# Kernel optimization log

Hardware: AMD Instinct MI355X
Metric: run time of the kernel (lower is better)

The kernel has to match this reference:

```python
import jax, jax.numpy as jnp
import numpy as np

TOPK = 5
POWER = 1.01


def setup_inputs() -> dict:
    key = jax.random.key(0)
    k1, k2 = jax.random.split(key)
    B, C = 16384, 8192
    inp = jax.random.normal(k1, (B, C), dtype=jnp.float32)
    target = jax.random.randint(k2, (B,), 0, C, dtype=jnp.int64 if jax.config.jax_enable_x64 else jnp.int32)
    return {"input": inp, "target": target}


def reference(input, target):
    B = input.shape[0]
    rows = jnp.arange(B)
    # log(softmax(x)) == log_softmax(x)
    log_prob = jax.nn.log_softmax(input, axis=-1)  # [B, C]
    # top-k selection over classes
    topk_vals, topk_idx = jax.lax.top_k(input, TOPK)  # [B, K]
    # custom power-based softmax on the top-k subset
    exp_in = jnp.power(jnp.asarray(POWER, input.dtype), topk_vals)  # [B, K]
    log_prob_topk = jnp.log(exp_in / jnp.sum(exp_in, axis=-1, keepdims=True))
    # scatter the top-k log-probs back into a copy of log_prob
    log_prob_copy = log_prob.at[rows[:, None], topk_idx].set(log_prob_topk)
    # gather-based cross-entropy terms
    loss1 = jnp.mean(-log_prob[rows, target])
    loss2 = jnp.mean(-log_prob_copy[rows, target])
    return loss1 + loss2
```

## Files before the change

### kernel.cpp

```cpp
#include <hip/hip_runtime.h>

#define BLOCK 256
#define NCHUNK 8
#define NC 8192

typedef float f4 __attribute__((ext_vector_type(4)));

__device__ __forceinline__ float fexp2(float x) { return __builtin_amdgcn_exp2f(x); }
__device__ __forceinline__ float flog2(float x) { return __builtin_amdgcn_logf(x); }

__device__ __forceinline__ void cas(float& hi, float& lo) {
    float h = fmaxf(hi, lo), l = fminf(hi, lo);
    hi = h; lo = l;
}

__device__ __forceinline__ void sort5(float& a0, float& a1, float& a2, float& a3, float& a4) {
    cas(a0, a1); cas(a3, a4); cas(a2, a4); cas(a2, a3); cas(a1, a4);
    cas(a0, a3); cas(a0, a2); cas(a1, a3); cas(a1, a2);
}

__device__ __forceinline__ void merge55(float& a0, float& a1, float& a2, float& a3, float& a4,
                                        float b0, float b1, float b2, float b3, float b4) {
    float L0 = fmaxf(a0, b4);
    float L1 = fmaxf(a1, b3);
    float L2 = fmaxf(a2, b2);
    float L3 = fmaxf(a3, b1);
    float L4 = fmaxf(a4, b0);
    sort5(L0, L1, L2, L3, L4);
    a0 = L0; a1 = L1; a2 = L2; a3 = L3; a4 = L4;
}

__global__ __launch_bounds__(BLOCK, 6) void ce_topk_rows(const float* __restrict__ inp,
                                                         const int* __restrict__ target,
                                                         float* __restrict__ row_loss) {
    constexpr float LOG2E  = 1.4426950408889634f;
    constexpr float LN2    = 0.6931471805599453f;
    constexpr float LN_P   = 0.009950330853155723f;
    constexpr float LOG2_P = 0.014355292977070041f;
    const float NI = -__builtin_inff();

    const int row  = blockIdx.x;
    const int tid  = threadIdx.x;
    const int lane = tid & 63;
    const int wav  = tid >> 6;
    const float* rp = inp + (size_t)row * NC;

    __shared__ float wsum[4];
    __shared__ float wtop[4][5];

    float xt = 0.f;
    if (tid == 0) xt = rp[target[row]];

    f4 c[NCHUNK];
    #pragma unroll
    for (int j = 0; j < NCHUNK; ++j)
        c[j] = reinterpret_cast<const f4*>(rp)[tid + BLOCK * j];

    float es = 0.f;
    float a0, a1, a2, a3, a4;

    {
        float v0 = c[0][0], v1 = c[0][1], v2 = c[0][2], v3 = c[0][3];
        es = (fexp2(v0 * LOG2E) + fexp2(v1 * LOG2E))
           + (fexp2(v2 * LOG2E) + fexp2(v3 * LOG2E));
        cas(v0, v1); cas(v2, v3); cas(v0, v2); cas(v1, v3); cas(v1, v2);
        a0 = v0; a1 = v1; a2 = v2; a3 = v3; a4 = NI;
    }

    #pragma unroll
    for (int j = 1; j < NCHUNK; ++j) {
        float v0 = c[j][0], v1 = c[j][1], v2 = c[j][2], v3 = c[j][3];
        es += (fexp2(v0 * LOG2E) + fexp2(v1 * LOG2E))
            + (fexp2(v2 * LOG2E) + fexp2(v3 * LOG2E));
        cas(v0, v1); cas(v2, v3); cas(v0, v2); cas(v1, v3); cas(v1, v2);
        a1 = fmaxf(a1, v3);
        a2 = fmaxf(a2, v2);
        a3 = fmaxf(a3, v1);
        a4 = fmaxf(a4, v0);
        sort5(a0, a1, a2, a3, a4);
    }

    #pragma unroll
    for (int o = 32; o > 0; o >>= 1) es += __shfl_xor(es, o, 64);

    #pragma unroll
    for (int o = 1; o < 64; o <<= 1) {
        float b0 = __shfl_xor(a0, o, 64);
        float b1 = __shfl_xor(a1, o, 64);
        float b2 = __shfl_xor(a2, o, 64);
        float b3 = __shfl_xor(a3, o, 64);
        float b4 = __shfl_xor(a4, o, 64);
        merge55(a0, a1, a2, a3, a4, b0, b1, b2, b3, b4);
    }

    if (lane == 0) {
        wsum[wav] = es;
        wtop[wav][0] = a0; wtop[wav][1] = a1; wtop[wav][2] = a2;
        wtop[wav][3] = a3; wtop[wav][4] = a4;
    }
    __syncthreads();

    if (tid == 0) {
        float s = wsum[0] + wsum[1] + wsum[2] + wsum[3];
        float A0 = wtop[0][0], A1 = wtop[0][1], A2 = wtop[0][2], A3 = wtop[0][3], A4 = wtop[0][4];
        #pragma unroll
        for (int w = 1; w < 4; ++w)
            merge55(A0, A1, A2, A3, A4,
                    wtop[w][0], wtop[w][1], wtop[w][2], wtop[w][3], wtop[w][4]);

        float spsum = fexp2(A0 * LOG2_P) + fexp2(A1 * LOG2_P) + fexp2(A2 * LOG2_P)
                    + fexp2(A3 * LOG2_P) + fexp2(A4 * LOG2_P);

        float lse  = LN2 * flog2(s);
        float l1   = lse - xt;
        float lsep = LN2 * flog2(spsum);
        bool found = (xt >= A4);
        float l2   = found ? (lsep - xt * LN_P) : l1;
        row_loss[row] = l1 + l2;
    }
}

__global__ __launch_bounds__(1024) void ce_topk_reduce(const float* __restrict__ rl,
                                                       float* __restrict__ out, int B) {
    float acc = 0.f;
    const float4* r4 = (const float4*)rl;
    const int n4 = B / 4;
    for (int i = threadIdx.x; i < n4; i += 1024) {
        float4 v = r4[i];
        acc += (v.x + v.y) + (v.z + v.w);
    }
    #pragma unroll
    for (int o = 32; o > 0; o >>= 1) acc += __shfl_xor(acc, o, 64);
    __shared__ float sr[16];
    if ((threadIdx.x & 63) == 0) sr[threadIdx.x >> 6] = acc;
    __syncthreads();
    if (threadIdx.x == 0) {
        float s = 0.f;
        #pragma unroll
        for (int w = 0; w < 16; ++w) s += sr[w];
        out[0] = s / (float)B;
    }
}

extern "C" void kernel_launch(void* const* d_in, const int* in_sizes, int n_in,
                              void* d_out, int out_size, void* d_ws, size_t ws_size,
                              hipStream_t stream) {
    const float* inp = (const float*)d_in[0];
    const int*   tgt = (const int*)d_in[1];
    const int B = in_sizes[1];
    float* rl = (float*)d_ws;
    ce_topk_rows<<<B, BLOCK, 0, stream>>>(inp, tgt, rl);
    ce_topk_reduce<<<1, 1024, 0, stream>>>(rl, (float*)d_out, B);
}
```

Before: 100.2 us.

## Process one row per wavefront with rolling register prefetch pipeline

Each 64-lane wavefront now handles a whole row, so a block of 256 threads covers four rows and the LDS exchange and __syncthreads are gone. Each lane streams 32 float4 chunks through an 8-deep register ring that issues the next load while the current chunk is processed. The aim is to remove the block-level synchronisation and cross-wave merge, and to keep more loads in flight per wave. In exchange each wave does more serial work per row, and occupancy depends on register pressure under the new launch bounds.

Result: no change. 102.0 us (+1.8%).

```diff
diff --git a/kernel.cpp b/kernel.cpp
--- a/kernel.cpp
+++ b/kernel.cpp
@@ -1,8 +1,8 @@
 #include <hip/hip_runtime.h>
 
-#define BLOCK 256
-#define NCHUNK 8
 #define NC 8192
+#define NCHUNK 32
+#define DEPTH 8
 
 typedef float f4 __attribute__((ext_vector_type(4)));
 
@@ -30,37 +30,33 @@
     a0 = L0; a1 = L1; a2 = L2; a3 = L3; a4 = L4;
 }
 
-__global__ __launch_bounds__(BLOCK, 6) void ce_topk_rows(const float* __restrict__ inp,
-                                                         const int* __restrict__ target,
-                                                         float* __restrict__ row_loss) {
+__global__ __launch_bounds__(256, 8) void ce_topk_rows(const float* __restrict__ inp,
+                                                       const int* __restrict__ target,
+                                                       float* __restrict__ row_loss) {
     constexpr float LOG2E  = 1.4426950408889634f;
     constexpr float LN2    = 0.6931471805599453f;
     constexpr float LN_P   = 0.009950330853155723f;
     constexpr float LOG2_P = 0.014355292977070041f;
     const float NI = -__builtin_inff();
 
-    const int row  = blockIdx.x;
-    const int tid  = threadIdx.x;
-    const int lane = tid & 63;
-    const int wav  = tid >> 6;
+    const int lane = threadIdx.x & 63;
+    const int row  = (blockIdx.x << 2) | (threadIdx.x >> 6);
     const float* rp = inp + (size_t)row * NC;
+    const f4* p = reinterpret_cast<const f4*>(rp) + lane;
 
-    __shared__ float wsum[4];
-    __shared__ float wtop[4][5];
+    f4 c[DEPTH];
+    #pragma unroll
+    for (int i = 0; i < DEPTH; ++i) c[i] = p[64 * i];
 
-    float xt = 0.f;
-    if (tid == 0) xt = rp[target[row]];
-
-    f4 c[NCHUNK];
-    #pragma unroll
-    for (int j = 0; j < NCHUNK; ++j)
-        c[j] = reinterpret_cast<const f4*>(rp)[tid + BLOCK * j];
+    const int   tgt = target[row];
+    const float xt  = rp[tgt];
 
     float es = 0.f;
     float a0, a1, a2, a3, a4;
 
     {
         float v0 = c[0][0], v1 = c[0][1], v2 = c[0][2], v3 = c[0][3];
+        c[0] = p[64 * DEPTH];
         es = (fexp2(v0 * LOG2E) + fexp2(v1 * LOG2E))
            + (fexp2(v2 * LOG2E) + fexp2(v3 * LOG2E));
         cas(v0, v1); cas(v2, v3); cas(v0, v2); cas(v1, v3); cas(v1, v2);
@@ -68,8 +64,9 @@
     }
 
     #pragma unroll
-    for (int j = 1; j < NCHUNK; ++j) {
-        float v0 = c[j][0], v1 = c[j][1], v2 = c[j][2], v3 = c[j][3];
+    for (int i = 1; i < NCHUNK; ++i) {
+        float v0 = c[i & 7][0], v1 = c[i & 7][1], v2 = c[i & 7][2], v3 = c[i & 7][3];
+        if (i + DEPTH < NCHUNK) c[i & 7] = p[64 * (i + DEPTH)];
         es += (fexp2(v0 * LOG2E) + fexp2(v1 * LOG2E))
             + (fexp2(v2 * LOG2E) + fexp2(v3 * LOG2E));
         cas(v0, v1); cas(v2, v3); cas(v0, v2); cas(v1, v3); cas(v1, v2);
@@ -94,27 +91,12 @@
     }
 
     if (lane == 0) {
-        wsum[wav] = es;
-        wtop[wav][0] = a0; wtop[wav][1] = a1; wtop[wav][2] = a2;
-        wtop[wav][3] = a3; wtop[wav][4] = a4;
-    }
-    __syncthreads();
-
-    if (tid == 0) {
-        float s = wsum[0] + wsum[1] + wsum[2] + wsum[3];
-        float A0 = wtop[0][0], A1 = wtop[0][1], A2 = wtop[0][2], A3 = wtop[0][3], A4 = wtop[0][4];
-        #pragma unroll
-        for (int w = 1; w < 4; ++w)
-            merge55(A0, A1, A2, A3, A4,
-                    wtop[w][0], wtop[w][1], wtop[w][2], wtop[w][3], wtop[w][4]);
-
-        float spsum = fexp2(A0 * LOG2_P) + fexp2(A1 * LOG2_P) + fexp2(A2 * LOG2_P)
-                    + fexp2(A3 * LOG2_P) + fexp2(A4 * LOG2_P);
-
-        float lse  = LN2 * flog2(s);
+        float spsum = fexp2(a0 * LOG2_P) + fexp2(a1 * LOG2_P) + fexp2(a2 * LOG2_P)
+                    + fexp2(a3 * LOG2_P) + fexp2(a4 * LOG2_P);
+        float lse  = LN2 * flog2(es);
         float l1   = lse - xt;
         float lsep = LN2 * flog2(spsum);
-        bool found = (xt >= A4);
+        bool found = (xt >= a4);
         float l2   = found ? (lsep - xt * LN_P) : l1;
         row_loss[row] = l1 + l2;
     }
@@ -149,6 +131,6 @@
     const int*   tgt = (const int*)d_in[1];
     const int B = in_sizes[1];
     float* rl = (float*)d_ws;
-    ce_topk_rows<<<B, BLOCK, 0, stream>>>(inp, tgt, rl);
+    ce_topk_rows<<<B / 4, 256, 0, stream>>>(inp, tgt, rl);
     ce_topk_reduce<<<1, 1024, 0, stream>>>(rl, (float*)d_out, B);
 }
```
